# Kernel tuning notes

Hardware: AMD Instinct MI355X
Metric: run time of the kernel (lower is better)

Reference implementation:

```python
import jax, jax.numpy as jnp
import numpy as np

B = 16384
IN = 1024
H = 1024
LN_EPS = 1e-5


def setup_inputs() -> dict:
    key = jax.random.key(0)
    ks = jax.random.split(key, 8)
    # Five gate Linears fused into one weight [IN+H, 5H] (order: f, i, o, c, m)
    scale = 1.0 / np.sqrt(IN + H)
    W = jax.random.uniform(ks[0], (IN + H, 5 * H), jnp.float32, -scale, scale)
    b = jax.random.uniform(ks[1], (5 * H,), jnp.float32, -scale, scale)
    return {
        "x": jax.random.normal(ks[2], (B, IN), jnp.float32),
        "h_prev": jax.random.normal(ks[3], (B, H), jnp.float32),
        "c_prev": jax.random.normal(ks[4], (B, H), jnp.float32),
        "W": W,
        "b": b,
        "ln_gamma": jnp.ones((H,), jnp.float32),
        "ln_beta": jnp.zeros((H,), jnp.float32),
        "retention": jnp.full((H,), 0.9, jnp.float32),
    }


def _layernorm(z, gamma, beta):
    mu = jnp.mean(z, axis=-1, keepdims=True)
    var = jnp.var(z, axis=-1, keepdims=True)
    return (z - mu) * jax.lax.rsqrt(var + LN_EPS) * gamma + beta


def reference(x, h_prev, c_prev, W, b, ln_gamma, ln_beta, retention):
    combined = jnp.concatenate([x, h_prev], axis=-1)        # [B, IN+H]
    gates = combined @ W + b                                # [B, 5H] fused GEMM
    f_pre, i_pre, o_pre, c_pre_act, m_pre = jnp.split(gates, 5, axis=-1)
    f_gate = jax.nn.sigmoid(f_pre)
    i_gate = jax.nn.sigmoid(i_pre)
    o_gate = jax.nn.sigmoid(o_pre)
    c_cand = jnp.tanh(c_pre_act)
    m_gate = jax.nn.sigmoid(m_pre)
    c_new = f_gate * c_prev + i_gate * c_cand
    c_new = c_new * retention + (1.0 - retention) * c_prev
    c_new = m_gate * c_new + (1.0 - m_gate) * c_prev
    # exp(ln)/(1+exp(ln)) == sigmoid(layernorm(o_gate))
    o_exp = jax.nn.sigmoid(_layernorm(o_gate, ln_gamma, ln_beta))
    h_new = o_exp * jnp.tanh(c_new)
    return h_new, c_new
```

## Files before the change

kernel.cpp:

```cpp
#include <hip/hip_runtime.h>
#include <math.h>


typedef unsigned short u16;
typedef unsigned int   u32;
typedef short  short8 __attribute__((ext_vector_type(8)));
typedef float  f32x4  __attribute__((ext_vector_type(4)));
typedef u16    u16x4  __attribute__((ext_vector_type(4)));
typedef u32    u32x4  __attribute__((ext_vector_type(4)));

#define B_ROWS 16384
#define K_DIM  2048
#define N_DIM  5120
#define H_DIM  1024

__device__ __forceinline__ float b2f(u16 u) {
    u32 v = ((u32)u) << 16;
    return __uint_as_float(v);
}
__device__ __forceinline__ u16 f2b(float f) {
    u32 x = __float_as_uint(f);
    u32 r = (x + 0x7fffu + ((x >> 16) & 1u)) >> 16;
    return (u16)r;
}
__device__ __forceinline__ float sigm(float v) {
    return 1.f / (1.f + __expf(-v));
}
__device__ __forceinline__ float tanh_fast(float v) {
    v = fminf(fmaxf(v, -15.f), 15.f);
    float e = __expf(-2.f * v);
    return (1.f - e) / (1.f + e);
}

__global__ __launch_bounds__(256) void convert_A(const float* __restrict__ x,
                                                 const float* __restrict__ h,
                                                 u16* __restrict__ A) {
    size_t idx = ((size_t)blockIdx.x * 256 + threadIdx.x) * 8;
    int row = (int)(idx >> 11);
    int col = (int)(idx & 2047);
    const float* src = (col < 1024) ? (x + (size_t)row * 1024 + col)
                                    : (h + (size_t)row * 1024 + (col - 1024));
    f32x4 v0 = *(const f32x4*)src;
    f32x4 v1 = *(const f32x4*)(src + 4);
    u32x4 w;
    w.x = (u32)f2b(v0.x) | ((u32)f2b(v0.y) << 16);
    w.y = (u32)f2b(v0.z) | ((u32)f2b(v0.w) << 16);
    w.z = (u32)f2b(v1.x) | ((u32)f2b(v1.y) << 16);
    w.w = (u32)f2b(v1.z) | ((u32)f2b(v1.w) << 16);
    *(u32x4*)(A + idx) = w;
}

__global__ __launch_bounds__(256) void convert_W(const float* __restrict__ W,
                                                 u16* __restrict__ Wt) {
    __shared__ float tile[32][33];
    int tx = threadIdx.x & 31;
    int ty = threadIdx.x >> 5;
    int n0 = blockIdx.x * 32;
    int k0 = blockIdx.y * 32;
#pragma unroll
    for (int i = 0; i < 4; ++i)
        tile[ty + 8 * i][tx] = W[(size_t)(k0 + ty + 8 * i) * N_DIM + n0 + tx];
    __syncthreads();
#pragma unroll
    for (int i = 0; i < 4; ++i)
        Wt[(size_t)(n0 + ty + 8 * i) * K_DIM + k0 + tx] = f2b(tile[tx][ty + 8 * i]);
}

#define BM 128
#define BN 128
#define BK 64

__device__ __forceinline__ void gld_lds16(const void* g, void* l) {
    __builtin_amdgcn_global_load_lds(
        (const __attribute__((address_space(1))) void*)g,
        (__attribute__((address_space(3))) void*)l, 16, 0, 0);
}

__global__ __launch_bounds__(256, 2) void gemm_gates(const u16* __restrict__ A,
                                                     const u16* __restrict__ Bt,
                                                     const float* __restrict__ bias,
                                                     u16* __restrict__ gates) {
    __shared__ u16 As[BM * BK];
    __shared__ u16 Bs[BN * BK];

    const int t  = threadIdx.x;
    const int m0 = blockIdx.x * BM;
    const int n0 = blockIdx.y * BN;
    const int l  = t & 63;
    const int wid = t >> 6;
    const int wm = (wid >> 1) << 6;
    const int wn = (wid & 1) << 6;
    const int lr = l & 15;
    const int lh = l >> 4;

    f32x4 acc[4][4] = {};

    const int sRow = t >> 3;
    const int sK   = (t & 7) * 8;
    const u16* aPtr = A  + (size_t)(m0 + sRow) * K_DIM + sK;
    const u16* bPtr = Bt + (size_t)(n0 + sRow) * K_DIM + sK;

    for (int ktile = 0; ktile < K_DIM / BK; ++ktile) {
#pragma unroll
        for (int it = 0; it < 4; ++it) {
            gld_lds16(aPtr + (size_t)it * 32 * K_DIM, &As[(it * 256 + t) * 8]);
            gld_lds16(bPtr + (size_t)it * 32 * K_DIM, &Bs[(it * 256 + t) * 8]);
        }
        __syncthreads();
#pragma unroll
        for (int s = 0; s < 2; ++s) {
            short8 af[4], bf[4];
#pragma unroll
            for (int mi = 0; mi < 4; ++mi)
                af[mi] = *(const short8*)&As[(wm + mi * 16 + lr) * BK + s * 32 + lh * 8];
#pragma unroll
            for (int ni = 0; ni < 4; ++ni)
                bf[ni] = *(const short8*)&Bs[(wn + ni * 16 + lr) * BK + s * 32 + lh * 8];
#pragma unroll
            for (int mi = 0; mi < 4; ++mi)
#pragma unroll
                for (int ni = 0; ni < 4; ++ni)
                    acc[mi][ni] = __builtin_amdgcn_mfma_f32_16x16x32_bf16(
                        af[mi], bf[ni], acc[mi][ni], 0, 0, 0);
        }
        __syncthreads();
        aPtr += BK;
        bPtr += BK;
    }

    const int grp = n0 >> 10;
#pragma unroll
    for (int ni = 0; ni < 4; ++ni) {
        int col = n0 + wn + ni * 16 + lr;
        float bv = bias[col];
#pragma unroll
        for (int mi = 0; mi < 4; ++mi) {
#pragma unroll
            for (int j = 0; j < 4; ++j) {
                int row = m0 + wm + mi * 16 + lh * 4 + j;
                float v = acc[mi][ni][j] + bv;
                float g = (grp == 3) ? tanh_fast(v) : sigm(v);
                gates[(size_t)row * N_DIM + col] = f2b(g);
            }
        }
    }
}

__global__ __launch_bounds__(256) void fuse_out(const u16* __restrict__ gates,
                                                const float* __restrict__ c_prev,
                                                const float* __restrict__ ret,
                                                const float* __restrict__ gamma,
                                                const float* __restrict__ beta,
                                                float* __restrict__ out) {
    const int r = blockIdx.x;
    const int t = threadIdx.x;
    const u16* g = gates + (size_t)r * N_DIM;
    const int j0 = t * 4;

    u16x4 ov = *(const u16x4*)(g + 2048 + j0);
    float o0 = b2f(ov.x), o1 = b2f(ov.y), o2 = b2f(ov.z), o3 = b2f(ov.w);
    float s1 = o0 + o1 + o2 + o3;
    float s2 = o0 * o0 + o1 * o1 + o2 * o2 + o3 * o3;
#pragma unroll
    for (int off = 32; off; off >>= 1) {
        s1 += __shfl_xor(s1, off, 64);
        s2 += __shfl_xor(s2, off, 64);
    }
    __shared__ float red[8];
    if ((t & 63) == 0) { red[t >> 6] = s1; red[4 + (t >> 6)] = s2; }
    __syncthreads();
    float S1 = red[0] + red[1] + red[2] + red[3];
    float S2 = red[4] + red[5] + red[6] + red[7];
    float mu   = S1 * (1.f / 1024.f);
    float var  = S2 * (1.f / 1024.f) - mu * mu;
    float rstd = rsqrtf(var + 1e-5f);

    u16x4 fv = *(const u16x4*)(g + j0);
    u16x4 iv = *(const u16x4*)(g + 1024 + j0);
    u16x4 cv = *(const u16x4*)(g + 3072 + j0);
    u16x4 mv = *(const u16x4*)(g + 4096 + j0);
    f32x4 cp = *(const f32x4*)(c_prev + (size_t)r * H_DIM + j0);
    f32x4 rt = *(const f32x4*)(ret + j0);
    f32x4 gm = *(const f32x4*)(gamma + j0);
    f32x4 bt = *(const f32x4*)(beta + j0);

    float of[4] = {o0, o1, o2, o3};
    u16 fa[4] = {fv.x, fv.y, fv.z, fv.w};
    u16 ia[4] = {iv.x, iv.y, iv.z, iv.w};
    u16 ca[4] = {cv.x, cv.y, cv.z, cv.w};
    u16 ma[4] = {mv.x, mv.y, mv.z, mv.w};

    f32x4 hout, cout;
#pragma unroll
    for (int i = 0; i < 4; ++i) {
        float f = b2f(fa[i]), ig = b2f(ia[i]), cc = b2f(ca[i]), m = b2f(ma[i]);
        float cpv = cp[i], rv = rt[i];
        float c1 = f * cpv + ig * cc;
        float c2 = c1 * rv + (1.f - rv) * cpv;
        float cn = m * c2 + (1.f - m) * cpv;
        float ln = (of[i] - mu) * rstd * gm[i] + bt[i];
        float oe = sigm(ln);
        float hn = oe * tanh_fast(cn);
        hout[i] = hn;
        cout[i] = cn;
    }
    *(f32x4*)(out + (size_t)r * H_DIM + j0) = hout;
    *(f32x4*)(out + (size_t)B_ROWS * H_DIM + (size_t)r * H_DIM + j0) = cout;
}

extern "C" void kernel_launch(void* const* d_in, const int* in_sizes, int n_in,
                              void* d_out, int out_size, void* d_ws, size_t ws_size,
                              hipStream_t stream) {
    const float* x      = (const float*)d_in[0];
    const float* h_prev = (const float*)d_in[1];
    const float* c_prev = (const float*)d_in[2];
    const float* W      = (const float*)d_in[3];
    const float* bias   = (const float*)d_in[4];
    const float* gamma  = (const float*)d_in[5];
    const float* beta   = (const float*)d_in[6];
    const float* ret    = (const float*)d_in[7];
    float* out = (float*)d_out;

    u16* Abuf  = (u16*)d_ws;
    u16* Wt    = Abuf + (size_t)B_ROWS * K_DIM;
    u16* gates = Wt + (size_t)N_DIM * K_DIM;

    convert_A<<<(B_ROWS * K_DIM / 8) / 256, 256, 0, stream>>>(x, h_prev, Abuf);
    convert_W<<<dim3(N_DIM / 32, K_DIM / 32), 256, 0, stream>>>(W, Wt);
    gemm_gates<<<dim3(B_ROWS / BM, N_DIM / BN), 256, 0, stream>>>(Abuf, Wt, bias, gates);
    fuse_out<<<B_ROWS, 256, 0, stream>>>(gates, c_prev, ret, gamma, beta, out);
}
```

Measured before the change: 523.0 us.

## Enlarge GEMM tiles to 256x256 with a 4-stage LDS pipeline and block swizzle

The gates GEMM moves to 256x256 block tiles with 512 threads and BK=32. A 4-buffer LDS ring is prefetched three stages ahead, with manual vmcnt waits and a single barrier per k-step replacing the two syncthreads. A block-index swizzle groups nearby tiles for L2 reuse, and MFMA sections run at raised wave priority. The aim is to hide global-load latency and raise arithmetic intensity, at the cost of much more register pressure (128 accumulators per lane) and 128 KB of LDS, which may limit occupancy.

Result: no change. 517.9 us (-1.0%).

```diff
diff --git a/kernel.cpp b/kernel.cpp
--- a/kernel.cpp
+++ b/kernel.cpp
@@ -66,9 +66,8 @@
         Wt[(size_t)(n0 + ty + 8 * i) * K_DIM + k0 + tx] = f2b(tile[tx][ty + 8 * i]);
 }
 
-#define BM 128
-#define BN 128
-#define BK 64
+#define BK 32
+#define NBUF 4
 
 __device__ __forceinline__ void gld_lds16(const void* g, void* l) {
     __builtin_amdgcn_global_load_lds(
@@ -76,57 +75,85 @@
         (__attribute__((address_space(3))) void*)l, 16, 0, 0);
 }
 
-__global__ __launch_bounds__(256, 2) void gemm_gates(const u16* __restrict__ A,
+__global__ __launch_bounds__(512, 2) void gemm_gates(const u16* __restrict__ A,
                                                      const u16* __restrict__ Bt,
                                                      const float* __restrict__ bias,
                                                      u16* __restrict__ gates) {
-    __shared__ u16 As[BM * BK];
-    __shared__ u16 Bs[BN * BK];
-
-    const int t  = threadIdx.x;
-    const int m0 = blockIdx.x * BM;
-    const int n0 = blockIdx.y * BN;
-    const int l  = t & 63;
+    __shared__ u16 lds[NBUF][2][256 * BK];
+
+    const int t = threadIdx.x;
+    const int bid = blockIdx.x;
+    const int swz = (bid & 7) * 160 + (bid >> 3);
+    const int m0 = (swz & 63) << 8;
+    const int n0 = (swz >> 6) << 8;
+
+    const int l   = t & 63;
     const int wid = t >> 6;
-    const int wm = (wid >> 1) << 6;
-    const int wn = (wid & 1) << 6;
-    const int lr = l & 15;
-    const int lh = l >> 4;
-
-    f32x4 acc[4][4] = {};
-
-    const int sRow = t >> 3;
-    const int sK   = (t & 7) * 8;
-    const u16* aPtr = A  + (size_t)(m0 + sRow) * K_DIM + sK;
-    const u16* bPtr = Bt + (size_t)(n0 + sRow) * K_DIM + sK;
-
-    for (int ktile = 0; ktile < K_DIM / BK; ++ktile) {
-#pragma unroll
-        for (int it = 0; it < 4; ++it) {
-            gld_lds16(aPtr + (size_t)it * 32 * K_DIM, &As[(it * 256 + t) * 8]);
-            gld_lds16(bPtr + (size_t)it * 32 * K_DIM, &Bs[(it * 256 + t) * 8]);
+    const int wm  = (wid >> 2) << 7;
+    const int wn  = (wid & 3) << 6;
+    const int lr  = l & 15;
+    const int lh  = l >> 4;
+
+    f32x4 acc[8][4] = {};
+
+    const int sRow = t >> 2;
+    const int sCol = (t & 3) * 8;
+    const u16* aBase = A  + (size_t)(m0 + sRow) * K_DIM + sCol;
+    const u16* bBase = Bt + (size_t)(n0 + sRow) * K_DIM + sCol;
+    const int ldsOff = t * 8;
+
+#define STAGE(kt, buf)                                                        \
+    do {                                                                      \
+        const u16* a_ = aBase + (kt) * BK;                                    \
+        const u16* b_ = bBase + (kt) * BK;                                    \
+        gld_lds16(a_,                        &lds[buf][0][ldsOff]);           \
+        gld_lds16(a_ + (size_t)128 * K_DIM,  &lds[buf][0][ldsOff + 4096]);    \
+        gld_lds16(b_,                        &lds[buf][1][ldsOff]);           \
+        gld_lds16(b_ + (size_t)128 * K_DIM,  &lds[buf][1][ldsOff + 4096]);    \
+    } while (0)
+
+    STAGE(0, 0);
+    STAGE(1, 1);
+    STAGE(2, 2);
+    __builtin_amdgcn_sched_barrier(0);
+    asm volatile("s_waitcnt vmcnt(8)" ::: "memory");
+    __builtin_amdgcn_s_barrier();
+    __builtin_amdgcn_sched_barrier(0);
+
+    const int NKT = K_DIM / BK;
+    for (int kt = 0; kt < NKT; ++kt) {
+        const int buf = kt & (NBUF - 1);
+        if (kt + 3 < NKT) STAGE(kt + 3, (kt + 3) & (NBUF - 1));
+
+        const u16* As = lds[buf][0];
+        const u16* Bs = lds[buf][1];
+        short8 af[8], bf[4];
+#pragma unroll
+        for (int ni = 0; ni < 4; ++ni)
+            bf[ni] = *(const short8*)&Bs[(wn + ni * 16 + lr) * BK + lh * 8];
+#pragma unroll
+        for (int mi = 0; mi < 8; ++mi)
+            af[mi] = *(const short8*)&As[(wm + mi * 16 + lr) * BK + lh * 8];
+
+        __builtin_amdgcn_s_setprio(1);
+#pragma unroll
+        for (int mi = 0; mi < 8; ++mi)
+#pragma unroll
+            for (int ni = 0; ni < 4; ++ni)
+                acc[mi][ni] = __builtin_amdgcn_mfma_f32_16x16x32_bf16(
+                    af[mi], bf[ni], acc[mi][ni], 0, 0, 0);
+        __builtin_amdgcn_s_setprio(0);
+
+        __builtin_amdgcn_sched_barrier(0);
+        if (kt < NKT - 3) {
+            asm volatile("s_waitcnt vmcnt(8)" ::: "memory");
+        } else {
+            asm volatile("s_waitcnt vmcnt(0)" ::: "memory");
         }
-        __syncthreads();
-#pragma unroll
-        for (int s = 0; s < 2; ++s) {
-            short8 af[4], bf[4];
-#pragma unroll
-            for (int mi = 0; mi < 4; ++mi)
-                af[mi] = *(const short8*)&As[(wm + mi * 16 + lr) * BK + s * 32 + lh * 8];
-#pragma unroll
-            for (int ni = 0; ni < 4; ++ni)
-                bf[ni] = *(const short8*)&Bs[(wn + ni * 16 + lr) * BK + s * 32 + lh * 8];
-#pragma unroll
-            for (int mi = 0; mi < 4; ++mi)
-#pragma unroll
-                for (int ni = 0; ni < 4; ++ni)
-                    acc[mi][ni] = __builtin_amdgcn_mfma_f32_16x16x32_bf16(
-                        af[mi], bf[ni], acc[mi][ni], 0, 0, 0);
-        }
-        __syncthreads();
-        aPtr += BK;
-        bPtr += BK;
-    }
+        __builtin_amdgcn_s_barrier();
+        __builtin_amdgcn_sched_barrier(0);
+    }
+#undef STAGE
 
     const int grp = n0 >> 10;
 #pragma unroll
@@ -134,7 +161,7 @@
         int col = n0 + wn + ni * 16 + lr;
         float bv = bias[col];
 #pragma unroll
-        for (int mi = 0; mi < 4; ++mi) {
+        for (int mi = 0; mi < 8; ++mi) {
 #pragma unroll
             for (int j = 0; j < 4; ++j) {
                 int row = m0 + wm + mi * 16 + lh * 4 + j;
@@ -227,6 +254,6 @@
 
     convert_A<<<(B_ROWS * K_DIM / 8) / 256, 256, 0, stream>>>(x, h_prev, Abuf);
     convert_W<<<dim3(N_DIM / 32, K_DIM / 32), 256, 0, stream>>>(W, Wt);
-    gemm_gates<<<dim3(B_ROWS / BM, N_DIM / BN), 256, 0, stream>>>(Abuf, Wt, bias, gates);
+    gemm_gates<<<(B_ROWS / 256) * (N_DIM / 256), 512, 0, stream>>>(Abuf, Wt, bias, gates);
     fuse_out<<<B_ROWS, 256, 0, stream>>>(gates, c_prev, ret, gamma, beta, out);
 }
```
